# Performance work log

Hardware: AMD Instinct MI355X
Metric: run time of the kernel (lower is better)

Reference implementation:

```python
import jax, jax.numpy as jnp
import numpy as np
from jax import lax

DEPTH = 5
LEAF = 2 ** DEPTH          # 32
GATES = LEAF - 1           # 31
LATENT = 128
IN_SHAPE = (128, 8, 8)     # C, H, W after mixture reshape
OUT_FEAT = IN_SHAPE[0] * IN_SHAPE[1] * IN_SHAPE[2]  # 8192
BATCH = 512


def conv_t(x, w, b):
    # PyTorch ConvTranspose2d(k=4, s=2, p=1): weight layout [in, out, kh, kw].
    # Equivalent fwd conv: flip spatial dims, swap in/out, lhs_dilation=2, pad k-1-p=2.
    w_ = jnp.flip(w, (2, 3)).transpose(1, 0, 2, 3)  # [out, in, kh, kw]
    y = lax.conv_general_dilated(
        x, w_, window_strides=(1, 1), padding=((2, 2), (2, 2)),
        lhs_dilation=(2, 2), dimension_numbers=("NCHW", "OIHW", "NCHW"))
    return y + b[None, :, None, None]


def leaf_probs_fn(x, gw, gb):
    # gatings: [B, GATES]
    g = jax.nn.sigmoid(x @ gw + gb)
    dens = jnp.ones((x.shape[0], 1), dtype=x.dtype)  # root density
    start = 0
    for d in range(1, DEPTH + 1):
        n_par = 2 ** (d - 1)
        gp = lax.dynamic_slice_in_dim(g, start, n_par, axis=1)  # [B, n_par]
        # left child (odd node index) uses g, right child uses 1-g, interleaved.
        dens = jnp.stack([dens * gp, dens * (1.0 - gp)], axis=-1).reshape(x.shape[0], 2 * n_par)
        start += n_par
    return dens  # [B, LEAF]


def setup_inputs() -> dict:
    key = jax.random.key(0)
    ks = jax.random.split(key, 10)
    C = IN_SHAPE[0]
    inp = {
        "x": jax.random.normal(ks[0], (BATCH, LATENT), dtype=jnp.float32),
        # SoftTree gating params (kaiming-normal ~ N(0, sqrt(2/fan_in)) approx)
        "gw": jax.random.normal(ks[1], (LATENT, GATES), dtype=jnp.float32) * (2.0 / LATENT) ** 0.5,
        "gb": jnp.zeros((GATES,), dtype=jnp.float32),
        # constant projection leaves
        "z": jax.random.normal(ks[2], (OUT_FEAT, LEAF), dtype=jnp.float32),
        # ConvTranspose2d weights, PyTorch layout [in_ch, out_ch, kh, kw]
        "w1": jax.random.normal(ks[3], (C, 128, 4, 4), dtype=jnp.float32) * 0.02,
        "b1": jnp.zeros((128,), dtype=jnp.float32),
        "w2": jax.random.normal(ks[4], (128, 64, 4, 4), dtype=jnp.float32) * 0.02,
        "b2": jnp.zeros((64,), dtype=jnp.float32),
        "w3": jax.random.normal(ks[5], (64, 3, 4, 4), dtype=jnp.float32) * 0.02,
        "b3": jnp.zeros((3,), dtype=jnp.float32),
    }
    return inp


def reference(x, gw, gb, z, w1, b1, w2, b2, w3, b3):
    lp = leaf_probs_fn(x, gw, gb)              # [B, LEAF]
    out = lp @ z.T                              # [B, OUT_FEAT] == (z @ lp.T).T
    out = out.reshape(-1, *IN_SHAPE)            # [B, 128, 8, 8]
    out = jax.nn.relu(conv_t(out, w1, b1))      # [B, 128, 16, 16]
    out = jax.nn.relu(conv_t(out, w2, b2))      # [B, 64, 32, 32]
    out = conv_t(out, w3, b3)                   # [B, 3, 64, 64]
    return out
```

## Files before the change

kernel.cpp:

```cpp
#include <hip/hip_runtime.h>
#include <hip/hip_bf16.h>
#include <stdint.h>

using bf16 = __hip_bfloat16;
typedef __attribute__((ext_vector_type(8))) short bf16x8;
typedef __attribute__((ext_vector_type(4))) float f32x4;

#define BATCHN 512

__device__ __forceinline__ void gload_lds16(const void* g, void* l) {
  __builtin_amdgcn_global_load_lds(
      (const __attribute__((address_space(1))) uint32_t*)g,
      (__attribute__((address_space(3))) uint32_t*)l, 16, 0, 0);
}

__global__ void gate_kernel(const float* __restrict__ x, const float* __restrict__ gw,
                            const float* __restrict__ gb, float* __restrict__ lp) {
  __shared__ float xs[128];
  __shared__ float gs[32];
  const int b = blockIdx.x;
  const int t = threadIdx.x;
  xs[t] = x[b*128 + t];
  xs[t + 64] = x[b*128 + 64 + t];
  __syncthreads();
  if (t < 31) {
    float acc = gb[t];
    #pragma unroll 8
    for (int k = 0; k < 128; ++k) acc += xs[k] * gw[k*31 + t];
    gs[t] = 1.f / (1.f + __expf(-acc));
  }
  __syncthreads();
  if (t < 32) {
    float prob = 1.f;
    #pragma unroll
    for (int d = 1; d <= 5; ++d) {
      int i = t >> (6 - d);
      int node = (1 << (d - 1)) - 1 + i;
      float gv = gs[node];
      prob *= ((t >> (5 - d)) & 1) ? (1.f - gv) : gv;
    }
    lp[b*32 + t] = prob;
  }
}

__global__ void mixture_kernel(const float* __restrict__ z, const float* __restrict__ lp,
                               bf16* __restrict__ x1) {
  __shared__ float lps[64 * 32];
  const int s = blockIdx.x;
  const int h = s >> 3, w = s & 7;
  const int b0 = blockIdx.y * 64;
  const int t = threadIdx.x;
  const int c = t & 127;
  const int half = t >> 7;
  float4 zr[8];
  const float4* zp = (const float4*)(z + (size_t)(c * 64 + s) * 32);
  #pragma unroll
  for (int i = 0; i < 8; ++i) zr[i] = zp[i];
  #pragma unroll
  for (int i = 0; i < 8; ++i) lps[t + 256 * i] = lp[b0 * 32 + t + 256 * i];
  __syncthreads();
  for (int bs = 0; bs < 32; ++bs) {
    int bl = half * 32 + bs;
    const float4* lr = (const float4*)(lps + bl * 32);
    float acc = 0.f;
    #pragma unroll
    for (int i = 0; i < 8; ++i) {
      float4 l4 = lr[i];
      acc += zr[i].x * l4.x + zr[i].y * l4.y + zr[i].z * l4.z + zr[i].w * l4.w;
    }
    int b = b0 + bl;
    x1[((size_t)(b * 10 + h + 1) * 10 + (w + 1)) * 128 + c] = __float2bfloat16(acc);
  }
}

__global__ void zero_halo(bf16* __restrict__ buf, int H, int W, int C) {
  int idx = blockIdx.x * 256 + threadIdx.x;
  int nvec = C >> 3;
  int P = 2 * (W + 2) + 2 * H;
  int total = BATCHN * P * nvec;
  if (idx >= total) return;
  int cv = idx % nvec;
  int p = (idx / nvec) % P;
  int b = idx / (nvec * P);
  int row, col;
  if (p < W + 2) { row = 0; col = p; }
  else if (p < 2 * (W + 2)) { row = H + 1; col = p - (W + 2); }
  else { int q = p - 2 * (W + 2); row = 1 + (q >> 1); col = (q & 1) ? (W + 1) : 0; }
  float4 z4 = {0.f, 0.f, 0.f, 0.f};
  *(float4*)(buf + ((size_t)(b * (H + 2) + row) * (W + 2) + col) * C + cv * 8) = z4;
}

__global__ void wprep_kernel(const float* __restrict__ w, bf16* __restrict__ wt,
                             int IC, int OCr, int OCp) {
  int idx = blockIdx.x * 256 + threadIdx.x;
  int NC = IC / 32;
  int total = 16 * OCp * IC;
  if (idx >= total) return;
  int e = idx & 7;
  int t = idx >> 3;
  int oc = t % OCp; t /= OCp;
  int q = t & 3; t >>= 2;
  int c = t % NC; t /= NC;
  int tap = t & 3, p = t >> 2;
  int ic = c * 32 + q * 8 + e;
  int dy = tap >> 1, dx = tap & 1;
  int py = p >> 1, px = p & 1;
  const int ktab[2][2] = {{1, 3}, {2, 0}};
  int ky = ktab[py][dy], kx = ktab[px][dx];
  float v = 0.f;
  if (oc < OCr) v = w[((ic * OCr + oc) * 4 + ky) * 4 + kx];
  wt[idx] = __float2bfloat16(v);
}

template<int IC, int OCp, int OCr, int IH, int IW, int ROWS, int BN,
         int WAVES_M, int WAVES_N, int MI, int NI, bool RELU, bool FINAL>
__global__ __launch_bounds__(256, 2)
void convt_pipe(const bf16* __restrict__ xin, const bf16* __restrict__ wt,
                const float* __restrict__ bias, bf16* __restrict__ xout,
                float* __restrict__ fout) {
  constexpr int NC = IC / 32;
  constexpr int PLANES = NC * 4;
  constexpr int IH2 = IH + 2, IW2 = IW + 2;
  constexpr int OH2 = 2 * IH + 2, OW2 = 2 * IW + 2;
  constexpr int NPIX = (ROWS + 2) * IW2;
  constexpr int CHUNK = PLANES * BN * 8;
  constexpr int NP = CHUNK / 512;
  constexpr int BPI = IH / ROWS;
  constexpr int WM = MI * 16, WN = NI * 16;
  constexpr int LIW = (IW == 8 ? 3 : (IW == 16 ? 4 : 5));
  constexpr int ICV = IC / 8;
  __shared__ bf16 Alds[PLANES * NPIX * 8];
  __shared__ bf16 Blds[2][CHUNK];

  const int tid = threadIdx.x;
  const int wave = tid >> 6, lane = tid & 63;
  const int q = lane >> 4, li = lane & 15;
  const int wm = wave / WAVES_N, wn = wave % WAVES_N;
  const int img = blockIdx.x / BPI;
  const int tb = blockIdx.x % BPI;
  const int n0 = blockIdx.y * BN;

  const bf16* src = xin + ((size_t)img * IH2 + tb * ROWS) * IW2 * IC;
  for (int g = tid; g < NPIX * ICV; g += 256) {
    const int pix = g / ICV;
    const int gr = g % ICV;
    const float4 v = *(const float4*)(src + (size_t)g * 8);
    *(float4*)(&Alds[(gr * NPIX + pix) * 8]) = v;
  }

  auto prefetch = [&](int chunk, int buf) {
    #pragma unroll
    for (int j = 0; j < (NP + 3) / 4; ++j) {
      const int jj = wave + 4 * j;
      if (NP % 4 != 0 && jj >= NP) break;
      size_t gelem;
      if (BN == 64) {
        gelem = ((size_t)(chunk * PLANES + jj) * OCp + n0 + lane) * 8;
      } else {
        gelem = ((size_t)(chunk * PLANES + jj * 4) * OCp + lane) * 8;
      }
      gload_lds16(wt + gelem, &Blds[buf][jj * 512]);
    }
  };

  prefetch(0, 0);

  int cpix[MI];
  #pragma unroll
  for (int mi = 0; mi < MI; ++mi) {
    const int m = wm * WM + mi * 16 + li;
    cpix[mi] = ((m >> LIW) + 1) * IW2 + (m & (IW - 1)) + 1;
  }

  f32x4 acc[4][MI][NI];
  #pragma unroll
  for (int p = 0; p < 4; ++p)
    #pragma unroll
    for (int mi = 0; mi < MI; ++mi)
      #pragma unroll
      for (int nj = 0; nj < NI; ++nj)
        acc[p][mi][nj] = (f32x4){0.f, 0.f, 0.f, 0.f};

  __syncthreads();

  for (int chunk = 0; chunk < 16; ++chunk) {
    if (chunk < 15) prefetch(chunk + 1, (chunk + 1) & 1);
    const int p = chunk >> 2, tap = chunk & 3;
    const int py = p >> 1, px = p & 1;
    const int sh = ((tap >> 1) ? (py ? 1 : -1) * IW2 : 0) + ((tap & 1) ? (px ? 1 : -1) : 0);
    const bf16* Bb = Blds[chunk & 1];
    #pragma unroll
    for (int c = 0; c < NC; ++c) {
      bf16x8 bfr[NI];
      #pragma unroll
      for (int nj = 0; nj < NI; ++nj)
        bfr[nj] = *(const bf16x8*)(Bb + ((c * 4 + q) * BN + wn * WN + nj * 16 + li) * 8);
      #pragma unroll
      for (int mi = 0; mi < MI; ++mi) {
        const bf16x8 a = *(const bf16x8*)(Alds + ((c * 4 + q) * NPIX + cpix[mi] + sh) * 8);
        #pragma unroll
        for (int nj = 0; nj < NI; ++nj)
          acc[p][mi][nj] = __builtin_amdgcn_mfma_f32_16x16x32_bf16(a, bfr[nj], acc[p][mi][nj], 0, 0, 0);
      }
    }
    __syncthreads();
  }

  if (!FINAL) {
    #pragma unroll
    for (int p = 0; p < 4; ++p) {
      const int py = p >> 1, px = p & 1;
      #pragma unroll
      for (int nj = 0; nj < NI; ++nj) {
        const int oc = n0 + wn * WN + nj * 16 + li;
        const float bv = bias[oc];
        #pragma unroll
        for (int mi = 0; mi < MI; ++mi) {
          #pragma unroll
          for (int r = 0; r < 4; ++r) {
            const int pix = (wm * MI + mi) * 16 + q * 4 + r;
            const int y = tb * ROWS + (pix >> LIW), x = pix & (IW - 1);
            float v = acc[p][mi][nj][r] + bv;
            if (RELU) v = fmaxf(v, 0.f);
            xout[(((size_t)img * OH2 + 2 * y + py + 1) * OW2 + 2 * x + px + 1) * OCp + oc] =
                __float2bfloat16(v);
          }
        }
      }
    }
  } else {
    const int oc = li;
    if (oc < OCr) {
      const float bv = bias[oc];
      #pragma unroll
      for (int py = 0; py < 2; ++py)
        #pragma unroll
        for (int mi = 0; mi < MI; ++mi)
          #pragma unroll
          for (int r = 0; r < 4; ++r) {
            const int pix = (wm * MI + mi) * 16 + q * 4 + r;
            const int y = tb * ROWS + (pix >> LIW), x = pix & (IW - 1);
            float2 v2;
            v2.x = acc[py * 2 + 0][mi][0][r] + bv;
            v2.y = acc[py * 2 + 1][mi][0][r] + bv;
            *(float2*)(&fout[(((size_t)img * 3 + oc) * 64 + 2 * y + py) * 64 + 2 * x]) = v2;
          }
    }
  }
}

extern "C" void kernel_launch(void* const* d_in, const int* in_sizes, int n_in,
                              void* d_out, int out_size, void* d_ws, size_t ws_size,
                              hipStream_t stream) {
  const float* x  = (const float*)d_in[0];
  const float* gw = (const float*)d_in[1];
  const float* gb = (const float*)d_in[2];
  const float* z  = (const float*)d_in[3];
  const float* w1 = (const float*)d_in[4];
  const float* b1 = (const float*)d_in[5];
  const float* w2 = (const float*)d_in[6];
  const float* b2 = (const float*)d_in[7];
  const float* w3 = (const float*)d_in[8];
  const float* b3 = (const float*)d_in[9];
  float* out = (float*)d_out;

  char* w = (char*)d_ws;
  float* lp  = (float*)(w);
  bf16* x1  = (bf16*)(w + 65536);
  bf16* x2  = (bf16*)(w + 13172736);
  bf16* x3  = (bf16*)(w + 55640064);
  bf16* wt1 = (bf16*)(w + 131399680);
  bf16* wt2 = (bf16*)(w + 131923968);
  bf16* wt3 = (bf16*)(w + 132186112);

  zero_halo<<<(512*36*16 + 255) / 256, 256, 0, stream>>>(x1, 8, 8, 128);
  zero_halo<<<(512*68*16 + 255) / 256, 256, 0, stream>>>(x2, 16, 16, 128);
  zero_halo<<<(512*132*8 + 255) / 256, 256, 0, stream>>>(x3, 32, 32, 64);

  gate_kernel<<<512, 64, 0, stream>>>(x, gw, gb, lp);

  wprep_kernel<<<(16*128*128 + 255) / 256, 256, 0, stream>>>(w1, wt1, 128, 128, 128);
  wprep_kernel<<<(16*64*128 + 255) / 256, 256, 0, stream>>>(w2, wt2, 128, 64, 64);
  wprep_kernel<<<(16*16*64 + 255) / 256, 256, 0, stream>>>(w3, wt3, 64, 3, 16);

  mixture_kernel<<<dim3(64, 8), 256, 0, stream>>>(z, lp, x1);

  convt_pipe<128,128,128, 8, 8, 8, 64, 2,2, 2,2, true,false>
      <<<dim3(512, 2), 256, 0, stream>>>(x1, wt1, b1, x2, nullptr);
  convt_pipe<128, 64, 64,16,16, 8, 64, 2,2, 4,2, true,false>
      <<<dim3(1024, 1), 256, 0, stream>>>(x2, wt2, b2, x3, nullptr);
  convt_pipe< 64, 16,  3,32,32, 8, 16, 4,1, 4,1, false,true>
      <<<dim3(2048, 1), 256, 0, stream>>>(x3, wt3, b3, nullptr, out);
}
```

Baseline: 240.0 us.

## Load conv weights directly into registers with double buffering instead of LDS

Drops the LDS staging buffer for the weight (B) operand in the transposed-conv kernels. Each lane now loads its own weight fragments from global memory straight into registers, double-buffered across taps, which removes the per-chunk __syncthreads and the LDS round trip. This trades higher register pressure and redundant global/L2 reads across waves for less LDS traffic and fewer barriers. Launch-bound occupancy is also tuned per layer.

```diff
diff --git a/kernel.cpp b/kernel.cpp
--- a/kernel.cpp
+++ b/kernel.cpp
@@ -7,12 +7,6 @@
 typedef __attribute__((ext_vector_type(4))) float f32x4;
 
 #define BATCHN 512
-
-__device__ __forceinline__ void gload_lds16(const void* g, void* l) {
-  __builtin_amdgcn_global_load_lds(
-      (const __attribute__((address_space(1))) uint32_t*)g,
-      (__attribute__((address_space(3))) uint32_t*)l, 16, 0, 0);
-}
 
 __global__ void gate_kernel(const float* __restrict__ x, const float* __restrict__ gw,
                             const float* __restrict__ gb, float* __restrict__ lp) {
@@ -113,24 +107,21 @@
 }
 
 template<int IC, int OCp, int OCr, int IH, int IW, int ROWS, int BN,
-         int WAVES_M, int WAVES_N, int MI, int NI, bool RELU, bool FINAL>
-__global__ __launch_bounds__(256, 2)
-void convt_pipe(const bf16* __restrict__ xin, const bf16* __restrict__ wt,
-                const float* __restrict__ bias, bf16* __restrict__ xout,
-                float* __restrict__ fout) {
+         int WAVES_M, int WAVES_N, int MI, int NI, int MINW, bool RELU, bool FINAL>
+__global__ __launch_bounds__(256, MINW)
+void convt_reg(const bf16* __restrict__ xin, const bf16* __restrict__ wt,
+               const float* __restrict__ bias, bf16* __restrict__ xout,
+               float* __restrict__ fout) {
   constexpr int NC = IC / 32;
   constexpr int PLANES = NC * 4;
   constexpr int IH2 = IH + 2, IW2 = IW + 2;
   constexpr int OH2 = 2 * IH + 2, OW2 = 2 * IW + 2;
   constexpr int NPIX = (ROWS + 2) * IW2;
-  constexpr int CHUNK = PLANES * BN * 8;
-  constexpr int NP = CHUNK / 512;
   constexpr int BPI = IH / ROWS;
   constexpr int WM = MI * 16, WN = NI * 16;
   constexpr int LIW = (IW == 8 ? 3 : (IW == 16 ? 4 : 5));
   constexpr int ICV = IC / 8;
   __shared__ bf16 Alds[PLANES * NPIX * 8];
-  __shared__ bf16 Blds[2][CHUNK];
 
   const int tid = threadIdx.x;
   const int wave = tid >> 6, lane = tid & 63;
@@ -148,22 +139,7 @@
     *(float4*)(&Alds[(gr * NPIX + pix) * 8]) = v;
   }
 
-  auto prefetch = [&](int chunk, int buf) {
-    #pragma unroll
-    for (int j = 0; j < (NP + 3) / 4; ++j) {
-      const int jj = wave + 4 * j;
-      if (NP % 4 != 0 && jj >= NP) break;
-      size_t gelem;
-      if (BN == 64) {
-        gelem = ((size_t)(chunk * PLANES + jj) * OCp + n0 + lane) * 8;
-      } else {
-        gelem = ((size_t)(chunk * PLANES + jj * 4) * OCp + lane) * 8;
-      }
-      gload_lds16(wt + gelem, &Blds[buf][jj * 512]);
-    }
-  };
-
-  prefetch(0, 0);
+  const bf16* wtp = wt + (size_t)(n0 + wn * WN + li) * 8;
 
   int cpix[MI];
   #pragma unroll
@@ -181,29 +157,40 @@
       for (int nj = 0; nj < NI; ++nj)
         acc[p][mi][nj] = (f32x4){0.f, 0.f, 0.f, 0.f};
 
-  __syncthreads();
-
-  for (int chunk = 0; chunk < 16; ++chunk) {
-    if (chunk < 15) prefetch(chunk + 1, (chunk + 1) & 1);
+  bf16x8 b0[NC][NI], b1[NC][NI];
+
+  auto loadB = [&](int chunk, bf16x8 (&bfr)[NC][NI]) {
+    #pragma unroll
+    for (int c = 0; c < NC; ++c)
+      #pragma unroll
+      for (int nj = 0; nj < NI; ++nj)
+        bfr[c][nj] = *(const bf16x8*)(wtp + ((size_t)(chunk * PLANES + c * 4 + q) * OCp + nj * 16) * 8);
+  };
+  auto compute = [&](int chunk, bf16x8 (&bfr)[NC][NI]) {
     const int p = chunk >> 2, tap = chunk & 3;
     const int py = p >> 1, px = p & 1;
     const int sh = ((tap >> 1) ? (py ? 1 : -1) * IW2 : 0) + ((tap & 1) ? (px ? 1 : -1) : 0);
-    const bf16* Bb = Blds[chunk & 1];
     #pragma unroll
     for (int c = 0; c < NC; ++c) {
-      bf16x8 bfr[NI];
-      #pragma unroll
-      for (int nj = 0; nj < NI; ++nj)
-        bfr[nj] = *(const bf16x8*)(Bb + ((c * 4 + q) * BN + wn * WN + nj * 16 + li) * 8);
       #pragma unroll
       for (int mi = 0; mi < MI; ++mi) {
         const bf16x8 a = *(const bf16x8*)(Alds + ((c * 4 + q) * NPIX + cpix[mi] + sh) * 8);
         #pragma unroll
         for (int nj = 0; nj < NI; ++nj)
-          acc[p][mi][nj] = __builtin_amdgcn_mfma_f32_16x16x32_bf16(a, bfr[nj], acc[p][mi][nj], 0, 0, 0);
+          acc[p][mi][nj] = __builtin_amdgcn_mfma_f32_16x16x32_bf16(a, bfr[c][nj], acc[p][mi][nj], 0, 0, 0);
       }
     }
-    __syncthreads();
+  };
+
+  loadB(0, b0);
+  __syncthreads();
+
+  #pragma unroll
+  for (int cc = 0; cc < 16; cc += 2) {
+    loadB(cc + 1, b1);
+    compute(cc, b0);
+    if (cc + 2 < 16) loadB(cc + 2, b0);
+    compute(cc + 1, b1);
   }
 
   if (!FINAL) {
@@ -285,10 +272,10 @@
 
   mixture_kernel<<<dim3(64, 8), 256, 0, stream>>>(z, lp, x1);
 
-  convt_pipe<128,128,128, 8, 8, 8, 64, 2,2, 2,2, true,false>
+  convt_reg<128,128,128, 8, 8, 8, 64, 2,2, 2,2, 3, true,false>
       <<<dim3(512, 2), 256, 0, stream>>>(x1, wt1, b1, x2, nullptr);
-  convt_pipe<128, 64, 64,16,16, 8, 64, 2,2, 4,2, true,false>
+  convt_reg<128, 64, 64,16,16, 8, 64, 2,2, 4,2, 2, true,false>
       <<<dim3(1024, 1), 256, 0, stream>>>(x2, wt2, b2, x3, nullptr);
-  convt_pipe< 64, 16,  3,32,32, 8, 16, 4,1, 4,1, false,true>
+  convt_reg< 64, 16,  3,32,32, 8, 16, 4,1, 4,1, 4, false,true>
       <<<dim3(2048, 1), 256, 0, stream>>>(x3, wt3, b3, nullptr, out);
 }
```

Measured after the change: 292.3 us. 1.22x slower.
